# Optimization experiments

Hardware: AMD Instinct MI355X
Metric: run time of the kernel (lower is better)

Reference implementation:

```python
import jax, jax.numpy as jnp
import numpy as np

D = 20            # doc / proto-action feature dim (hard-coded via .view(slate_size, 20))
SLATE = 5
K = 100           # neighbors per slate element
N_DOCS = 1_000_000
HID = 256
SLOPE = 0.01      # F.leaky_relu default negative slope


def setup_inputs() -> dict:
    key = jax.random.key(0)
    ks = jax.random.split(key, 6)
    def lin_w(k, out_d, in_d):
        # kaiming-ish scale, matches torch Linear init magnitude roughly
        return jax.random.uniform(k, (out_d, in_d), jnp.float32, -1.0, 1.0) / np.sqrt(in_d)
    return {
        "input_state": jax.random.normal(ks[0], (D,), jnp.float32),
        "candidate_docs": jax.random.normal(ks[1], (N_DOCS, D), jnp.float32),
        "W1": lin_w(ks[2], HID, D),
        "b1": jnp.zeros((HID,), jnp.float32),
        "W2": lin_w(ks[3], HID, HID),
        "b2": jnp.zeros((HID,), jnp.float32),
        "W3": lin_w(ks[4], SLATE * D, HID),
        "b3": jnp.zeros((SLATE * D,), jnp.float32),
    }


def reference(input_state, candidate_docs, W1, b1, W2, b2, W3, b3):
    # --- actor policy net: Linear -> leaky_relu, x3 (leaky_relu also on output, as in source) ---
    x = input_state
    for W, b in ((W1, b1), (W2, b2), (W3, b3)):
        x = jax.nn.leaky_relu(x @ W.T + b, negative_slope=SLOPE)
    proto_slate = x.reshape(SLATE, D)                       # [slate, 20]

    # --- per-slate-element L2 distance to every candidate doc, vectorized ---
    # dists[s, n] = ||candidate_docs[n] - proto_slate[s]||_2
    diff = candidate_docs[None, :, :] - proto_slate[:, None, :]   # [slate, N, 20]
    dists = jnp.sqrt(jnp.sum(diff * diff, axis=-1))               # [slate, N]

    # top-k smallest distances (replaces full argsort + slice in the source)
    _, idx = jax.lax.top_k(-dists, K)                             # [slate, K]
    indices_tensor = idx.reshape(-1)                              # [slate*K], concat order as in source
    candidates_tensor = candidate_docs[indices_tensor]            # [slate*K, 20]
    return candidates_tensor, indices_tensor
```

## Files before the change

kernel.cpp:

```cpp
#include <hip/hip_runtime.h>
#include <stdint.h>

#define DDIM    20
#define SLATE   5
#define KSEL    100
#define HID     256
#define SAMPN   16384
#define NSH     8
#define SHCAP   1024
#define RCAP    8192
#define STP     128
#define OUT_IDX_OFF (SLATE * KSEL * DDIM)

#define WS_PROTO   0
#define WS_PROTOF  1024
#define WS_TP2     1536
#define WS_TM2     1556
#define WS_THI     1576
#define WS_SHCNT   1600
#define WS_STRICT  4160
#define WS_CNT2    6720
#define WS_ZEND    7040
#define WS_SKEYS   8192
#define WS_CAND    172032
#define WS_CAND2   335872
#define WS_STD2    499712
#define WS_STIX    540672
#define WS_STLEN   561152

__device__ __forceinline__ double dleaky(double x) { return x >= 0.0 ? x : 0.01 * x; }

__device__ __forceinline__ double calc_d2(const float* doc, const double* p) {
    double acc = 0.0;
#pragma unroll
    for (int i = 0; i < DDIM; ++i) {
        double d = (double)doc[i] - p[i];
        acc = fma(d, d, acc);
    }
    return acc;
}

__device__ __forceinline__ void load_doc(const float* __restrict__ docs,
                                         size_t n, float* doc) {
    const float4* dp = (const float4*)(docs + n * DDIM);
    float4 v0 = dp[0], v1 = dp[1], v2 = dp[2], v3 = dp[3], v4 = dp[4];
    doc[0] = v0.x; doc[1] = v0.y; doc[2] = v0.z; doc[3] = v0.w;
    doc[4] = v1.x; doc[5] = v1.y; doc[6] = v1.z; doc[7] = v1.w;
    doc[8] = v2.x; doc[9] = v2.y; doc[10] = v2.z; doc[11] = v2.w;
    doc[12] = v3.x; doc[13] = v3.y; doc[14] = v3.z; doc[15] = v3.w;
    doc[16] = v4.x; doc[17] = v4.y; doc[18] = v4.z; doc[19] = v4.w;
}

__device__ __forceinline__ int slate_use_primary(
    const unsigned* __restrict__ shardCnt, const unsigned* __restrict__ strictSh,
    int s) {
    unsigned strictTot = 0; bool ovf = false;
    for (int sh = 0; sh < NSH; ++sh) {
        if (shardCnt[(sh * SLATE + s) * 16] > SHCAP) ovf = true;
        strictTot += strictSh[(sh * SLATE + s) * 16];
    }
    return (strictTot >= KSEL) && !ovf;
}

__global__ __launch_bounds__(256) void mlp_kernel(
    const float* __restrict__ x0,
    const float* __restrict__ W1, const float* __restrict__ b1,
    const float* __restrict__ W2, const float* __restrict__ b2,
    const float* __restrict__ W3, const float* __restrict__ b3,
    double* __restrict__ proto, float* __restrict__ protof,
    unsigned* __restrict__ zeroBase) {
    __shared__ double xs[DDIM];
    __shared__ double h1[HID];
    __shared__ double h2[HID];
    int t = threadIdx.x;
    for (int i = t; i < 1360; i += 256) zeroBase[i] = 0u;
    if (t < DDIM) xs[t] = (double)x0[t];
    __syncthreads();
    {
        double acc = 0.0;
#pragma unroll
        for (int i = 0; i < DDIM; ++i) acc = fma(xs[i], (double)W1[t * DDIM + i], acc);
        acc += (double)b1[t];
        h1[t] = dleaky(acc);
    }
    __syncthreads();
    {
        double acc = 0.0;
        for (int i = 0; i < HID; ++i) acc = fma(h1[i], (double)W2[t * HID + i], acc);
        acc += (double)b2[t];
        h2[t] = dleaky(acc);
    }
    __syncthreads();
    if (t < SLATE * DDIM) {
        double acc = 0.0;
        for (int i = 0; i < HID; ++i) acc = fma(h2[i], (double)W3[t * HID + i], acc);
        acc += (double)b3[t];
        double v = dleaky(acc);
        proto[t] = v;
        protof[t] = (float)v;
    }
}

__global__ __launch_bounds__(256) void sample_keys_kernel(
    const float* __restrict__ docs, const double* __restrict__ proto,
    unsigned short* __restrict__ skeys, int N) {
    __shared__ double ps[SLATE * DDIM];
    int t = threadIdx.x;
    if (t < SLATE * DDIM) ps[t] = proto[t];
    __syncthreads();
    int i = blockIdx.x * 256 + t;
    if (i >= SAMPN || i >= N) return;
    float doc[DDIM];
    load_doc(docs, (size_t)i, doc);
#pragma unroll
    for (int s = 0; s < SLATE; ++s) {
        double d2 = calc_d2(doc, ps + s * DDIM);
        skeys[s * SAMPN + i] = (unsigned short)(__float_as_uint((float)d2) >> 16);
    }
}

__global__ __launch_bounds__(1024) void select_kernel(
    const unsigned short* __restrict__ skeys,
    unsigned short* __restrict__ Tp2, unsigned short* __restrict__ Tm2,
    unsigned short* __restrict__ Thi) {
    int s = blockIdx.x, t = threadIdx.x;
    int lane = t & 63, w = t >> 6;
    __shared__ unsigned wsum[2][16];
    const unsigned* kp = (const unsigned*)(skeys + (size_t)s * SAMPN);
    unsigned kw[8];
#pragma unroll
    for (int j = 0; j < 8; ++j) kw[j] = kp[j * 1024 + t];

    unsigned X10 = 0, X100 = 0;
    int buf = 0;
    for (int b = 15; b >= 0; --b) {
        unsigned p10 = X10 | (1u << b), p100 = X100 | (1u << b);
        int c10 = 0, c100 = 0;
#pragma unroll
        for (int j = 0; j < 8; ++j) {
            unsigned lo = kw[j] & 0xffffu, hi = kw[j] >> 16;
            c10  += (lo < p10)  + (hi < p10);
            c100 += (lo < p100) + (hi < p100);
        }
#pragma unroll
        for (int off = 32; off; off >>= 1) {
            c10  += __shfl_down(c10, off);
            c100 += __shfl_down(c100, off);
        }
        if (lane == 0) wsum[buf][w] = (unsigned)c10 | ((unsigned)c100 << 16);
        __syncthreads();
        unsigned t10 = 0, t100 = 0;
        for (int i = 0; i < 16; ++i) {
            unsigned v = wsum[buf][i];
            t10 += v & 0xffffu; t100 += v >> 16;
        }
        if ((int)t10 < 10)   X10 = p10;
        if ((int)t100 < 100) X100 = p100;
        buf ^= 1;
    }
    if (t == 0) {
        unsigned tp = X10 + 2u; if (tp > 65535u) tp = 65535u;
        Tp2[s] = (unsigned short)tp;
        Tm2[s] = (unsigned short)(X10 >= 2u ? X10 - 2u : 0u);
        Thi[s] = (unsigned short)X100;
    }
}

__global__ __launch_bounds__(256) void compact1_kernel(
    const float* __restrict__ docs, const float* __restrict__ protof,
    const unsigned short* __restrict__ Tp2, const unsigned short* __restrict__ Tm2,
    unsigned* __restrict__ shardCnt, unsigned* __restrict__ strictSh,
    unsigned* __restrict__ candIdx, int N) {
    __shared__ float psf[SLATE * DDIM];
    __shared__ unsigned short ktp[SLATE], ktm[SLATE];
    int t = threadIdx.x;
    if (t < SLATE * DDIM) psf[t] = protof[t];
    if (t < SLATE) { ktp[t] = Tp2[t]; ktm[t] = Tm2[t]; }
    __syncthreads();

    int n = blockIdx.x * 256 + t;
    bool dv = n < N;
    int lane = t & 63;
    int sh = blockIdx.x & (NSH - 1);

    float doc[DDIM];
    if (dv) load_doc(docs, (size_t)n, doc);
    else {
#pragma unroll
        for (int i = 0; i < DDIM; ++i) doc[i] = 0.f;
    }
    float acc[SLATE] = {0.f, 0.f, 0.f, 0.f, 0.f};
#pragma unroll
    for (int i = 0; i < DDIM; ++i) {
        float dvi = doc[i];
#pragma unroll
        for (int s = 0; s < SLATE; ++s) {
            float d = dvi - psf[s * DDIM + i];
            acc[s] = fmaf(d, d, acc[s]);
        }
    }
#pragma unroll
    for (int s = 0; s < SLATE; ++s) {
        unsigned k32 = __float_as_uint(acc[s]) >> 16;
        bool hit = dv && k32 <= (unsigned)ktp[s];
        unsigned long long ms = __ballot(dv && k32 <= (unsigned)ktm[s]);
        if (ms) {
            int ldr = __ffsll(ms) - 1;
            if (lane == ldr)
                atomicAdd(&strictSh[(sh * SLATE + s) * 16], (unsigned)__popcll(ms));
        }
        unsigned long long mh = __ballot(hit);
        if (mh) {
            int ldr = __ffsll(mh) - 1;
            unsigned base = 0;
            if (lane == ldr)
                base = atomicAdd(&shardCnt[(sh * SLATE + s) * 16], (unsigned)__popcll(mh));
            base = __shfl(base, ldr);
            if (hit) {
                unsigned pos = base + (unsigned)__popcll(mh & ((1ull << lane) - 1ull));
                if (pos < SHCAP)
                    candIdx[((size_t)(s * NSH + sh)) * SHCAP + pos] = (unsigned)n;
            }
        }
    }
}

__global__ __launch_bounds__(256) void compact2_kernel(
    const float* __restrict__ docs, const double* __restrict__ proto,
    const unsigned short* __restrict__ Thi,
    const unsigned* __restrict__ shardCnt, const unsigned* __restrict__ strictSh,
    unsigned* __restrict__ cnt2, unsigned* __restrict__ candIdx2, int N) {
    __shared__ int act[SLATE];
    __shared__ int anyAct;
    __shared__ double ps[SLATE * DDIM];
    __shared__ unsigned short kt[SLATE];
    int t = threadIdx.x;
    if (t == 0) {
        int any = 0;
        for (int s = 0; s < SLATE; ++s) {
            int a = slate_use_primary(shardCnt, strictSh, s) ? 0 : 1;
            act[s] = a; any |= a;
        }
        anyAct = any;
    }
    __syncthreads();
    if (!anyAct) return;

    if (t < SLATE) kt[t] = Thi[t];
    if (t < SLATE * DDIM) ps[t] = proto[t];
    __syncthreads();
    for (int n = blockIdx.x * 256 + t; n < N; n += gridDim.x * 256) {
        float doc[DDIM];
        load_doc(docs, (size_t)n, doc);
        for (int s = 0; s < SLATE; ++s) {
            if (!act[s]) continue;
            double d2 = calc_d2(doc, ps + s * DDIM);
            unsigned key = __float_as_uint((float)d2) >> 16;
            if (key <= (unsigned)kt[s]) {
                unsigned pos = atomicAdd(&cnt2[s * 16], 1u);
                if (pos < RCAP) candIdx2[(size_t)s * RCAP + pos] = (unsigned)n;
            }
        }
    }
}

__global__ __launch_bounds__(256) void shard_rank_kernel(
    const float* __restrict__ docs, const double* __restrict__ proto,
    const unsigned* __restrict__ shardCnt, const unsigned* __restrict__ strictSh,
    const unsigned* __restrict__ cnt2,
    const unsigned* __restrict__ candIdx, const unsigned* __restrict__ candIdx2,
    double* __restrict__ stD2, unsigned* __restrict__ stIx,
    unsigned* __restrict__ stLen, int N) {
    int sh = blockIdx.x, s = blockIdx.y;
    int t = threadIdx.x;
    __shared__ double ld[SHCAP];
    __shared__ unsigned li[SHCAP];
    __shared__ double ps[DDIM];
    __shared__ double outD2[KSEL];
    __shared__ unsigned outIx[KSEL];
    __shared__ unsigned c_s;
    __shared__ const unsigned* src_s;
    if (t < DDIM) ps[t] = proto[s * DDIM + t];
    if (t == 0) {
        if (slate_use_primary(shardCnt, strictSh, s)) {
            unsigned c = shardCnt[(sh * SLATE + s) * 16];
            if (c > SHCAP) c = SHCAP;
            c_s = c;
            src_s = candIdx + ((size_t)(s * NSH + sh)) * SHCAP;
        } else {
            unsigned c2 = cnt2[s * 16]; if (c2 > RCAP) c2 = RCAP;
            unsigned L = (c2 + NSH - 1) / NSH;
            unsigned lo = sh * L, hi = lo + L;
            if (lo > c2) lo = c2;
            if (hi > c2) hi = c2;
            c_s = hi - lo;
            src_s = candIdx2 + (size_t)s * RCAP + lo;
        }
    }
    __syncthreads();
    unsigned c = c_s;
    const unsigned* src = src_s;

    for (unsigned i = t; i < c; i += 256) {
        unsigned idx = src[i];
        li[i] = idx;
        float doc[DDIM];
        load_doc(docs, (size_t)idx, doc);
        ld[i] = calc_d2(doc, ps);
    }
    __syncthreads();

    for (unsigned e = t; e < c; e += 256) {
        double de = ld[e]; unsigned ie = li[e];
        unsigned rank = 0;
        for (unsigned j = 0; j < c; ++j) {
            double dj = ld[j]; unsigned ij = li[j];
            rank += (dj < de) || (dj == de && ij < ie);
        }
        if (rank < KSEL) { outD2[rank] = de; outIx[rank] = ie; }
    }
    __syncthreads();

    unsigned L = c < KSEL ? c : KSEL;
    size_t base = (size_t)(s * NSH + sh) * STP;
    for (unsigned r = t; r < L; r += 256) {
        stD2[base + r] = outD2[r];
        stIx[base + r] = outIx[r];
    }
    if (t == 0) stLen[s * NSH + sh] = L;
}

__global__ __launch_bounds__(1024) void merge_kernel(
    const float* __restrict__ docs,
    const double* __restrict__ stD2, const unsigned* __restrict__ stIx,
    const unsigned* __restrict__ stLen, float* __restrict__ out) {
    int s = blockIdx.x, t = threadIdx.x;
    __shared__ double md[NSH * KSEL];
    __shared__ unsigned mi[NSH * KSEL];
    __shared__ unsigned Ls[NSH], offs[NSH + 1];
    __shared__ unsigned sel[KSEL];
    if (t < NSH) Ls[t] = stLen[s * NSH + t];
    __syncthreads();
    if (t == 0) {
        unsigned o = 0;
        for (int sh = 0; sh < NSH; ++sh) { offs[sh] = o; o += Ls[sh]; }
        offs[NSH] = o;
    }
    __syncthreads();
    for (int sh = 0; sh < NSH; ++sh) {
        unsigned L = Ls[sh];
        for (unsigned i = t; i < L; i += 1024) {
            md[sh * KSEL + i] = stD2[(size_t)(s * NSH + sh) * STP + i];
            mi[sh * KSEL + i] = stIx[(size_t)(s * NSH + sh) * STP + i];
        }
    }
    __syncthreads();

    unsigned S = offs[NSH];
    for (unsigned e = t; e < S; e += 1024) {
        int sh = 0;
        while (e >= offs[sh + 1]) ++sh;
        unsigned i = e - offs[sh];
        double xd = md[sh * KSEL + i];
        unsigned xi = mi[sh * KSEL + i];
        unsigned rank = i;
        for (int so = 0; so < NSH; ++so) {
            if (so == sh) continue;
            unsigned lo = 0, hi = Ls[so];
            while (lo < hi) {
                unsigned mid = (lo + hi) >> 1;
                double dj = md[so * KSEL + mid];
                unsigned ij = mi[so * KSEL + mid];
                bool less = (dj < xd) || (dj == xd && ij < xi);
                if (less) lo = mid + 1; else hi = mid;
            }
            rank += lo;
        }
        if (rank < KSEL) sel[rank] = xi;
    }
    __syncthreads();

    if (t < KSEL) out[(size_t)OUT_IDX_OFF + s * KSEL + t] = (float)sel[t];
    for (int pos = t; pos < KSEL * DDIM; pos += 1024) {
        int r = pos / DDIM, c = pos % DDIM;
        out[((size_t)s * KSEL + r) * DDIM + c] = docs[(size_t)sel[r] * DDIM + c];
    }
}

extern "C" void kernel_launch(void* const* d_in, const int* in_sizes, int n_in,
                              void* d_out, int out_size, void* d_ws, size_t ws_size,
                              hipStream_t stream) {
    const float* x0   = (const float*)d_in[0];
    const float* docs = (const float*)d_in[1];
    const float* W1   = (const float*)d_in[2];
    const float* b1   = (const float*)d_in[3];
    const float* W2   = (const float*)d_in[4];
    const float* b2   = (const float*)d_in[5];
    const float* W3   = (const float*)d_in[6];
    const float* b3   = (const float*)d_in[7];
    int N = in_sizes[1] / DDIM;

    char* ws = (char*)d_ws;
    double*         proto    = (double*)(ws + WS_PROTO);
    float*          protof   = (float*)(ws + WS_PROTOF);
    unsigned short* Tp2      = (unsigned short*)(ws + WS_TP2);
    unsigned short* Tm2      = (unsigned short*)(ws + WS_TM2);
    unsigned short* Thi      = (unsigned short*)(ws + WS_THI);
    unsigned*       shardCnt = (unsigned*)(ws + WS_SHCNT);
    unsigned*       strictSh = (unsigned*)(ws + WS_STRICT);
    unsigned*       cnt2     = (unsigned*)(ws + WS_CNT2);
    unsigned short* skeys    = (unsigned short*)(ws + WS_SKEYS);
    unsigned*       candIdx  = (unsigned*)(ws + WS_CAND);
    unsigned*       candIdx2 = (unsigned*)(ws + WS_CAND2);
    double*         stD2     = (double*)(ws + WS_STD2);
    unsigned*       stIx     = (unsigned*)(ws + WS_STIX);
    unsigned*       stLen    = (unsigned*)(ws + WS_STLEN);

    mlp_kernel<<<1, 256, 0, stream>>>(x0, W1, b1, W2, b2, W3, b3,
                                      proto, protof, shardCnt);
    sample_keys_kernel<<<SAMPN / 256, 256, 0, stream>>>(docs, proto, skeys, N);
    select_kernel<<<SLATE, 1024, 0, stream>>>(skeys, Tp2, Tm2, Thi);

    int nb = (N + 255) / 256;
    compact1_kernel<<<nb, 256, 0, stream>>>(docs, protof, Tp2, Tm2,
                                            shardCnt, strictSh, candIdx, N);
    compact2_kernel<<<1024, 256, 0, stream>>>(docs, proto, Thi, shardCnt, strictSh,
                                              cnt2, candIdx2, N);
    shard_rank_kernel<<<dim3(NSH, SLATE), 256, 0, stream>>>(
        docs, proto, shardCnt, strictSh, cnt2, candIdx, candIdx2,
        stD2, stIx, stLen, N);
    merge_kernel<<<SLATE, 1024, 0, stream>>>(docs, stD2, stIx, stLen,
                                             (float*)d_out);
}
```

Measured before the change: 103.4 us.

## Fuse the seven-kernel pipeline into one cooperative persistent kernel with grid syncs

Replaces the chain of seven kernel launches (MLP, sampling, threshold select, two compaction passes, shard ranking, merge) with a single cooperative kernel. Phases are separated by grid.sync, and the shared memory for each phase is overlaid through a union. The MLP is recomputed redundantly in each sampling block so the separate single-block MLP launch disappears. Compaction becomes a grid-stride loop over a grid sized from the occupancy query, capped at 1024 blocks. This removes launch gaps and serial tiny kernels at the cost of grid-wide barriers, partial occupancy during the small phases, and a fallback path if the cooperative launch fails.

```diff
diff --git a/kernel.cpp b/kernel.cpp
--- a/kernel.cpp
+++ b/kernel.cpp
@@ -1,5 +1,8 @@
 #include <hip/hip_runtime.h>
+#include <hip/hip_cooperative_groups.h>
 #include <stdint.h>
+
+namespace cg = cooperative_groups;
 
 #define DDIM    20
 #define SLATE   5
@@ -61,6 +64,316 @@
     }
     return (strictTot >= KSEL) && !ovf;
 }
+
+
+struct SmMlp  { double xs[DDIM]; double h1[HID]; double h2[HID]; double ps[SLATE * DDIM]; };
+struct SmSel  { unsigned wsum[2][4]; };
+struct SmCmp  { float psf[SLATE * DDIM]; unsigned short ktp[SLATE]; unsigned short ktm[SLATE]; };
+struct SmRec  { double ps[SLATE * DDIM]; unsigned short kt[SLATE]; int act[SLATE]; int anyAct; };
+struct SmRank { double ld[SHCAP]; double outD2[KSEL]; double ps[DDIM];
+                unsigned li[SHCAP]; unsigned outIx[KSEL];
+                unsigned c; const unsigned* src; };
+struct SmMrg  { double md[NSH * KSEL]; unsigned mi[NSH * KSEL];
+                unsigned Ls[NSH]; unsigned offs[NSH + 1]; unsigned sel[KSEL]; };
+union SmU { SmMlp mlp; SmSel sel; SmCmp cmp; SmRec rec; SmRank rank; SmMrg mrg; };
+
+__global__ __launch_bounds__(256, 4) void fused_kernel(
+    const float* __restrict__ x0, const float* __restrict__ docs,
+    const float* __restrict__ W1, const float* __restrict__ b1,
+    const float* __restrict__ W2, const float* __restrict__ b2,
+    const float* __restrict__ W3, const float* __restrict__ b3,
+    double* __restrict__ proto, float* __restrict__ protof,
+    unsigned short* __restrict__ Tp2, unsigned short* __restrict__ Tm2,
+    unsigned short* __restrict__ Thi,
+    unsigned* __restrict__ shardCnt, unsigned* __restrict__ strictSh,
+    unsigned* __restrict__ cnt2, unsigned short* __restrict__ skeys,
+    unsigned* __restrict__ candIdx, unsigned* __restrict__ candIdx2,
+    double* __restrict__ stD2, unsigned* __restrict__ stIx,
+    unsigned* __restrict__ stLen, float* __restrict__ out, int N) {
+    cg::grid_group grid = cg::this_grid();
+    const int bid  = blockIdx.x;
+    const int t    = threadIdx.x;
+    const int nblk = gridDim.x;
+    __shared__ SmU sm;
+
+    if (bid < SAMPN / 256) {
+        SmMlp& M = sm.mlp;
+        if (t < DDIM) M.xs[t] = (double)x0[t];
+        __syncthreads();
+        {
+            double acc = 0.0;
+#pragma unroll
+            for (int i = 0; i < DDIM; ++i) acc = fma(M.xs[i], (double)W1[t * DDIM + i], acc);
+            acc += (double)b1[t];
+            M.h1[t] = dleaky(acc);
+        }
+        __syncthreads();
+        {
+            double acc = 0.0;
+            for (int i = 0; i < HID; ++i) acc = fma(M.h1[i], (double)W2[t * HID + i], acc);
+            acc += (double)b2[t];
+            M.h2[t] = dleaky(acc);
+        }
+        __syncthreads();
+        if (t < SLATE * DDIM) {
+            double acc = 0.0;
+            for (int i = 0; i < HID; ++i) acc = fma(M.h2[i], (double)W3[t * HID + i], acc);
+            acc += (double)b3[t];
+            double v = dleaky(acc);
+            M.ps[t] = v;
+            if (bid == 0) { proto[t] = v; protof[t] = (float)v; }
+        }
+        __syncthreads();
+        int i = bid * 256 + t;
+        if (i < N) {
+            float doc[DDIM];
+            load_doc(docs, (size_t)i, doc);
+#pragma unroll
+            for (int s = 0; s < SLATE; ++s) {
+                double d2 = calc_d2(doc, M.ps + s * DDIM);
+                skeys[s * SAMPN + i] = (unsigned short)(__float_as_uint((float)d2) >> 16);
+            }
+        }
+    } else if (bid == SAMPN / 256) {
+        for (int i = t; i < 1360; i += 256) shardCnt[i] = 0u;
+    }
+    grid.sync();
+
+    if (bid < SLATE) {
+        const int s = bid, lane = t & 63, w = t >> 6;
+        const unsigned* kp = (const unsigned*)(skeys + (size_t)s * SAMPN);
+        unsigned kw[32];
+#pragma unroll
+        for (int j = 0; j < 32; ++j) kw[j] = kp[j * 256 + t];
+
+        unsigned X10 = 0, X100 = 0;
+        int buf = 0;
+        for (int b = 15; b >= 0; --b) {
+            unsigned p10 = X10 | (1u << b), p100 = X100 | (1u << b);
+            int c10 = 0, c100 = 0;
+#pragma unroll
+            for (int j = 0; j < 32; ++j) {
+                unsigned lo = kw[j] & 0xffffu, hi = kw[j] >> 16;
+                c10  += (lo < p10)  + (hi < p10);
+                c100 += (lo < p100) + (hi < p100);
+            }
+#pragma unroll
+            for (int off = 32; off; off >>= 1) {
+                c10  += __shfl_down(c10, off);
+                c100 += __shfl_down(c100, off);
+            }
+            if (lane == 0) sm.sel.wsum[buf][w] = (unsigned)c10 | ((unsigned)c100 << 16);
+            __syncthreads();
+            unsigned t10 = 0, t100 = 0;
+            for (int i = 0; i < 4; ++i) {
+                unsigned v = sm.sel.wsum[buf][i];
+                t10 += v & 0xffffu; t100 += v >> 16;
+            }
+            if ((int)t10 < 10)   X10 = p10;
+            if ((int)t100 < 100) X100 = p100;
+            buf ^= 1;
+        }
+        if (t == 0) {
+            unsigned tp = X10 + 2u; if (tp > 65535u) tp = 65535u;
+            Tp2[s] = (unsigned short)tp;
+            Tm2[s] = (unsigned short)(X10 >= 2u ? X10 - 2u : 0u);
+            Thi[s] = (unsigned short)X100;
+        }
+    }
+    grid.sync();
+
+    {
+        SmCmp& C = sm.cmp;
+        if (t < SLATE * DDIM) C.psf[t] = protof[t];
+        if (t < SLATE) { C.ktp[t] = Tp2[t]; C.ktm[t] = Tm2[t]; }
+        __syncthreads();
+        const int lane = t & 63;
+        const int sh = bid & (NSH - 1);
+        for (int base = bid * 256; base < N; base += nblk * 256) {
+            int n = base + t;
+            bool dv = n < N;
+            float doc[DDIM];
+            if (dv) load_doc(docs, (size_t)n, doc);
+            else {
+#pragma unroll
+                for (int i = 0; i < DDIM; ++i) doc[i] = 0.f;
+            }
+            float acc[SLATE] = {0.f, 0.f, 0.f, 0.f, 0.f};
+#pragma unroll
+            for (int i = 0; i < DDIM; ++i) {
+                float dvi = doc[i];
+#pragma unroll
+                for (int s = 0; s < SLATE; ++s) {
+                    float d = dvi - C.psf[s * DDIM + i];
+                    acc[s] = fmaf(d, d, acc[s]);
+                }
+            }
+#pragma unroll
+            for (int s = 0; s < SLATE; ++s) {
+                unsigned k32 = __float_as_uint(acc[s]) >> 16;
+                bool hit = dv && k32 <= (unsigned)C.ktp[s];
+                unsigned long long ms = __ballot(dv && k32 <= (unsigned)C.ktm[s]);
+                if (ms) {
+                    int ldr = __ffsll(ms) - 1;
+                    if (lane == ldr)
+                        atomicAdd(&strictSh[(sh * SLATE + s) * 16], (unsigned)__popcll(ms));
+                }
+                unsigned long long mh = __ballot(hit);
+                if (mh) {
+                    int ldr = __ffsll(mh) - 1;
+                    unsigned base2 = 0;
+                    if (lane == ldr)
+                        base2 = atomicAdd(&shardCnt[(sh * SLATE + s) * 16], (unsigned)__popcll(mh));
+                    base2 = __shfl(base2, ldr);
+                    if (hit) {
+                        unsigned pos = base2 + (unsigned)__popcll(mh & ((1ull << lane) - 1ull));
+                        if (pos < SHCAP)
+                            candIdx[((size_t)(s * NSH + sh)) * SHCAP + pos] = (unsigned)n;
+                    }
+                }
+            }
+        }
+    }
+    grid.sync();
+
+    {
+        SmRec& R = sm.rec;
+        if (t == 0) {
+            int any = 0;
+            for (int s = 0; s < SLATE; ++s) {
+                int a = slate_use_primary(shardCnt, strictSh, s) ? 0 : 1;
+                R.act[s] = a; any |= a;
+            }
+            R.anyAct = any;
+        }
+        __syncthreads();
+        if (R.anyAct) {
+            if (t < SLATE) R.kt[t] = Thi[t];
+            if (t < SLATE * DDIM) R.ps[t] = proto[t];
+            __syncthreads();
+            for (int n = bid * 256 + t; n < N; n += nblk * 256) {
+                float doc[DDIM];
+                load_doc(docs, (size_t)n, doc);
+                for (int s = 0; s < SLATE; ++s) {
+                    if (!R.act[s]) continue;
+                    double d2 = calc_d2(doc, R.ps + s * DDIM);
+                    unsigned key = __float_as_uint((float)d2) >> 16;
+                    if (key <= (unsigned)R.kt[s]) {
+                        unsigned pos = atomicAdd(&cnt2[s * 16], 1u);
+                        if (pos < RCAP) candIdx2[(size_t)s * RCAP + pos] = (unsigned)n;
+                    }
+                }
+            }
+            grid.sync();
+        }
+    }
+
+    if (bid < NSH * SLATE) {
+        const int sh = bid & (NSH - 1), s = bid >> 3;
+        SmRank& K = sm.rank;
+        if (t < DDIM) K.ps[t] = proto[s * DDIM + t];
+        if (t == 0) {
+            if (slate_use_primary(shardCnt, strictSh, s)) {
+                unsigned c = shardCnt[(sh * SLATE + s) * 16];
+                if (c > SHCAP) c = SHCAP;
+                K.c = c;
+                K.src = candIdx + ((size_t)(s * NSH + sh)) * SHCAP;
+            } else {
+                unsigned c2 = cnt2[s * 16]; if (c2 > RCAP) c2 = RCAP;
+                unsigned L = (c2 + NSH - 1) / NSH;
+                unsigned lo = sh * L, hi = lo + L;
+                if (lo > c2) lo = c2;
+                if (hi > c2) hi = c2;
+                K.c = hi - lo;
+                K.src = candIdx2 + (size_t)s * RCAP + lo;
+            }
+        }
+        __syncthreads();
+        unsigned c = K.c;
+        const unsigned* src = K.src;
+
+        for (unsigned i = t; i < c; i += 256) {
+            unsigned idx = src[i];
+            K.li[i] = idx;
+            float doc[DDIM];
+            load_doc(docs, (size_t)idx, doc);
+            K.ld[i] = calc_d2(doc, K.ps);
+        }
+        __syncthreads();
+
+        for (unsigned e = t; e < c; e += 256) {
+            double de = K.ld[e]; unsigned ie = K.li[e];
+            unsigned rank = 0;
+            for (unsigned j = 0; j < c; ++j) {
+                double dj = K.ld[j]; unsigned ij = K.li[j];
+                rank += (dj < de) || (dj == de && ij < ie);
+            }
+            if (rank < KSEL) { K.outD2[rank] = de; K.outIx[rank] = ie; }
+        }
+        __syncthreads();
+
+        unsigned L = c < KSEL ? c : KSEL;
+        size_t base = (size_t)(s * NSH + sh) * STP;
+        for (unsigned r = t; r < L; r += 256) {
+            stD2[base + r] = K.outD2[r];
+            stIx[base + r] = K.outIx[r];
+        }
+        if (t == 0) stLen[s * NSH + sh] = L;
+    }
+    grid.sync();
+
+    if (bid < SLATE) {
+        const int s = bid;
+        SmMrg& G = sm.mrg;
+        if (t < NSH) G.Ls[t] = stLen[s * NSH + t];
+        __syncthreads();
+        if (t == 0) {
+            unsigned o = 0;
+            for (int sh = 0; sh < NSH; ++sh) { G.offs[sh] = o; o += G.Ls[sh]; }
+            G.offs[NSH] = o;
+        }
+        __syncthreads();
+        for (int sh = 0; sh < NSH; ++sh) {
+            unsigned L = G.Ls[sh];
+            for (unsigned i = t; i < L; i += 256) {
+                G.md[sh * KSEL + i] = stD2[(size_t)(s * NSH + sh) * STP + i];
+                G.mi[sh * KSEL + i] = stIx[(size_t)(s * NSH + sh) * STP + i];
+            }
+        }
+        __syncthreads();
+
+        unsigned S = G.offs[NSH];
+        for (unsigned e = t; e < S; e += 256) {
+            int sh = 0;
+            while (e >= G.offs[sh + 1]) ++sh;
+            unsigned i = e - G.offs[sh];
+            double xd = G.md[sh * KSEL + i];
+            unsigned xi = G.mi[sh * KSEL + i];
+            unsigned rank = i;
+            for (int so = 0; so < NSH; ++so) {
+                if (so == sh) continue;
+                unsigned lo = 0, hi = G.Ls[so];
+                while (lo < hi) {
+                    unsigned mid = (lo + hi) >> 1;
+                    double dj = G.md[so * KSEL + mid];
+                    unsigned ij = G.mi[so * KSEL + mid];
+                    bool less = (dj < xd) || (dj == xd && ij < xi);
+                    if (less) lo = mid + 1; else hi = mid;
+                }
+                rank += lo;
+            }
+            if (rank < KSEL) G.sel[rank] = xi;
+        }
+        __syncthreads();
+
+        if (t < KSEL) out[(size_t)OUT_IDX_OFF + s * KSEL + t] = (float)G.sel[t];
+        for (int pos = t; pos < KSEL * DDIM; pos += 256) {
+            int r = pos / DDIM, c = pos % DDIM;
+            out[((size_t)s * KSEL + r) * DDIM + c] = docs[(size_t)G.sel[r] * DDIM + c];
+        }
+    }
+}
+
 
 __global__ __launch_bounds__(256) void mlp_kernel(
     const float* __restrict__ x0,
@@ -415,20 +728,61 @@
     double*         stD2     = (double*)(ws + WS_STD2);
     unsigned*       stIx     = (unsigned*)(ws + WS_STIX);
     unsigned*       stLen    = (unsigned*)(ws + WS_STLEN);
-
-    mlp_kernel<<<1, 256, 0, stream>>>(x0, W1, b1, W2, b2, W3, b3,
-                                      proto, protof, shardCnt);
-    sample_keys_kernel<<<SAMPN / 256, 256, 0, stream>>>(docs, proto, skeys, N);
-    select_kernel<<<SLATE, 1024, 0, stream>>>(skeys, Tp2, Tm2, Thi);
-
-    int nb = (N + 255) / 256;
-    compact1_kernel<<<nb, 256, 0, stream>>>(docs, protof, Tp2, Tm2,
-                                            shardCnt, strictSh, candIdx, N);
-    compact2_kernel<<<1024, 256, 0, stream>>>(docs, proto, Thi, shardCnt, strictSh,
-                                              cnt2, candIdx2, N);
-    shard_rank_kernel<<<dim3(NSH, SLATE), 256, 0, stream>>>(
-        docs, proto, shardCnt, strictSh, cnt2, candIdx, candIdx2,
-        stD2, stIx, stLen, N);
-    merge_kernel<<<SLATE, 1024, 0, stream>>>(docs, stD2, stIx, stLen,
-                                             (float*)d_out);
-}
+    float*          outp     = (float*)d_out;
+
+    static int g_nblk = -1;
+    if (g_nblk == -1) {
+        int per_cu = 0;
+        if (hipOccupancyMaxActiveBlocksPerMultiprocessor(&per_cu, fused_kernel, 256, 0)
+                != hipSuccess || per_cu <= 0)
+            per_cu = 0;
+        int ncu = 256;
+        int dev = 0;
+        hipDeviceProp_t prop;
+        if (hipGetDevice(&dev) == hipSuccess &&
+            hipGetDeviceProperties(&prop, dev) == hipSuccess &&
+            prop.multiProcessorCount > 0)
+            ncu = prop.multiProcessorCount;
+        long cap = (long)per_cu * (long)ncu;
+        int nb = cap >= 1024 ? 1024 : (int)cap;
+        nb &= ~7;
+        g_nblk = (nb >= 72) ? nb : 0;
+    }
+
+    bool done = false;
+    if (g_nblk > 0) {
+        void* args[] = { (void*)&x0, (void*)&docs, (void*)&W1, (void*)&b1,
+                         (void*)&W2, (void*)&b2, (void*)&W3, (void*)&b3,
+                         (void*)&proto, (void*)&protof,
+                         (void*)&Tp2, (void*)&Tm2, (void*)&Thi,
+                         (void*)&shardCnt, (void*)&strictSh, (void*)&cnt2,
+                         (void*)&skeys, (void*)&candIdx, (void*)&candIdx2,
+                         (void*)&stD2, (void*)&stIx, (void*)&stLen,
+                         (void*)&outp, (void*)&N };
+        hipError_t e = hipLaunchCooperativeKernel((const void*)fused_kernel,
+                                                  dim3(g_nblk), dim3(256),
+                                                  args, 0, stream);
+        if (e == hipSuccess) {
+            done = true;
+        } else {
+            (void)hipGetLastError();
+            g_nblk = 0;
+        }
+    }
+
+    if (!done) {
+        mlp_kernel<<<1, 256, 0, stream>>>(x0, W1, b1, W2, b2, W3, b3,
+                                          proto, protof, shardCnt);
+        sample_keys_kernel<<<SAMPN / 256, 256, 0, stream>>>(docs, proto, skeys, N);
+        select_kernel<<<SLATE, 1024, 0, stream>>>(skeys, Tp2, Tm2, Thi);
+        int nb = (N + 255) / 256;
+        compact1_kernel<<<nb, 256, 0, stream>>>(docs, protof, Tp2, Tm2,
+                                                shardCnt, strictSh, candIdx, N);
+        compact2_kernel<<<1024, 256, 0, stream>>>(docs, proto, Thi, shardCnt, strictSh,
+                                                  cnt2, candIdx2, N);
+        shard_rank_kernel<<<dim3(NSH, SLATE), 256, 0, stream>>>(
+            docs, proto, shardCnt, strictSh, cnt2, candIdx, candIdx2,
+            stD2, stIx, stLen, N);
+        merge_kernel<<<SLATE, 1024, 0, stream>>>(docs, stD2, stIx, stLen, outp);
+    }
+}
```

Measured after the change: 329.3 us. 218% more time.

## Fuse MLP with sampling and merge rank stages into one per-slate kernel

Applied to the files above, without the earlier changes.

Each sampling block now recomputes the MLP redundantly so the separate MLP launch disappears, with an extra block doing the counter zeroing. The fallback full-scan compaction, the per-shard ranking and the merge are replaced by one 1024-thread kernel per slate. It gathers all primary candidates and ranks them with a chunked all-pairs comparison, templated on how many candidates each thread owns. This cuts launches and global round-trips, but every block repeats the MLP work, and the fallback path now scans all N docs from only 5 blocks.

```diff
diff --git a/kernel.cpp b/kernel.cpp
--- a/kernel.cpp
+++ b/kernel.cpp
@@ -1,5 +1,6 @@
 #include <hip/hip_runtime.h>
 #include <stdint.h>
+#include <math.h>
 
 #define DDIM    20
 #define SLATE   5
@@ -9,7 +10,7 @@
 #define NSH     8
 #define SHCAP   1024
 #define RCAP    8192
-#define STP     128
+#define CHUNK   2048
 #define OUT_IDX_OFF (SLATE * KSEL * DDIM)
 
 #define WS_PROTO   0
@@ -24,9 +25,6 @@
 #define WS_SKEYS   8192
 #define WS_CAND    172032
 #define WS_CAND2   335872
-#define WS_STD2    499712
-#define WS_STIX    540672
-#define WS_STLEN   561152
 
 __device__ __forceinline__ double dleaky(double x) { return x >= 0.0 ? x : 0.01 * x; }
 
@@ -62,18 +60,22 @@
     return (strictTot >= KSEL) && !ovf;
 }
 
-__global__ __launch_bounds__(256) void mlp_kernel(
-    const float* __restrict__ x0,
+__global__ __launch_bounds__(256) void mlp_sample_kernel(
+    const float* __restrict__ x0, const float* __restrict__ docs,
     const float* __restrict__ W1, const float* __restrict__ b1,
     const float* __restrict__ W2, const float* __restrict__ b2,
     const float* __restrict__ W3, const float* __restrict__ b3,
     double* __restrict__ proto, float* __restrict__ protof,
-    unsigned* __restrict__ zeroBase) {
+    unsigned short* __restrict__ skeys, unsigned* __restrict__ zeroBase, int N) {
+    const int bid = blockIdx.x, t = threadIdx.x;
+    if (bid == SAMPN / 256) {
+        for (int i = t; i < 1360; i += 256) zeroBase[i] = 0u;
+        return;
+    }
     __shared__ double xs[DDIM];
     __shared__ double h1[HID];
     __shared__ double h2[HID];
-    int t = threadIdx.x;
-    for (int i = t; i < 1360; i += 256) zeroBase[i] = 0u;
+    __shared__ double ps[SLATE * DDIM];
     if (t < DDIM) xs[t] = (double)x0[t];
     __syncthreads();
     {
@@ -96,26 +98,19 @@
         for (int i = 0; i < HID; ++i) acc = fma(h2[i], (double)W3[t * HID + i], acc);
         acc += (double)b3[t];
         double v = dleaky(acc);
-        proto[t] = v;
-        protof[t] = (float)v;
-    }
-}
-
-__global__ __launch_bounds__(256) void sample_keys_kernel(
-    const float* __restrict__ docs, const double* __restrict__ proto,
-    unsigned short* __restrict__ skeys, int N) {
-    __shared__ double ps[SLATE * DDIM];
-    int t = threadIdx.x;
-    if (t < SLATE * DDIM) ps[t] = proto[t];
-    __syncthreads();
-    int i = blockIdx.x * 256 + t;
-    if (i >= SAMPN || i >= N) return;
-    float doc[DDIM];
-    load_doc(docs, (size_t)i, doc);
-#pragma unroll
-    for (int s = 0; s < SLATE; ++s) {
-        double d2 = calc_d2(doc, ps + s * DDIM);
-        skeys[s * SAMPN + i] = (unsigned short)(__float_as_uint((float)d2) >> 16);
+        ps[t] = v;
+        if (bid == 0) { proto[t] = v; protof[t] = (float)v; }
+    }
+    __syncthreads();
+    int i = bid * 256 + t;
+    if (i < SAMPN && i < N) {
+        float doc[DDIM];
+        load_doc(docs, (size_t)i, doc);
+#pragma unroll
+        for (int s = 0; s < SLATE; ++s) {
+            double d2 = calc_d2(doc, ps + s * DDIM);
+            skeys[s * SAMPN + i] = (unsigned short)(__float_as_uint((float)d2) >> 16);
+        }
     }
 }
 
@@ -225,165 +220,117 @@
     }
 }
 
-__global__ __launch_bounds__(256) void compact2_kernel(
+template<int NOWN>
+__device__ __forceinline__ void rank_select(
+    const float* __restrict__ docs, const unsigned* __restrict__ lst,
+    unsigned ctot, const double* ps, double* ld, unsigned* li,
+    unsigned* outIx, int t) {
+    double   myD2[NOWN];
+    unsigned myIx[NOWN];
+    unsigned myRank[NOWN];
+#pragma unroll
+    for (int k = 0; k < NOWN; ++k) {
+        unsigned e = (unsigned)t + 1024u * (unsigned)k;
+        myD2[k] = INFINITY; myIx[k] = 0xffffffffu; myRank[k] = 0u;
+        if (e < ctot) {
+            unsigned idx = lst[e];
+            float doc[DDIM];
+            load_doc(docs, (size_t)idx, doc);
+            myIx[k] = idx;
+            myD2[k] = calc_d2(doc, ps);
+        }
+    }
+    for (unsigned c0 = 0; c0 < ctot; c0 += CHUNK) {
+        unsigned cn = (ctot - c0) < CHUNK ? (ctot - c0) : CHUNK;
+        __syncthreads();
+        for (unsigned j = t; j < cn; j += 1024) {
+            unsigned idx = lst[c0 + j];
+            float doc[DDIM];
+            load_doc(docs, (size_t)idx, doc);
+            li[j] = idx;
+            ld[j] = calc_d2(doc, ps);
+        }
+        __syncthreads();
+        for (unsigned j = 0; j < cn; ++j) {
+            double dj = ld[j]; unsigned ij = li[j];
+#pragma unroll
+            for (int k = 0; k < NOWN; ++k)
+                myRank[k] += ((dj < myD2[k]) || (dj == myD2[k] && ij < myIx[k])) ? 1u : 0u;
+        }
+    }
+    __syncthreads();
+#pragma unroll
+    for (int k = 0; k < NOWN; ++k)
+        if (myRank[k] < KSEL) outIx[myRank[k]] = myIx[k];
+}
+
+__global__ __launch_bounds__(1024) void rank_merge_kernel(
     const float* __restrict__ docs, const double* __restrict__ proto,
     const unsigned short* __restrict__ Thi,
     const unsigned* __restrict__ shardCnt, const unsigned* __restrict__ strictSh,
-    unsigned* __restrict__ cnt2, unsigned* __restrict__ candIdx2, int N) {
-    __shared__ int act[SLATE];
-    __shared__ int anyAct;
-    __shared__ double ps[SLATE * DDIM];
-    __shared__ unsigned short kt[SLATE];
-    int t = threadIdx.x;
-    if (t == 0) {
-        int any = 0;
-        for (int s = 0; s < SLATE; ++s) {
-            int a = slate_use_primary(shardCnt, strictSh, s) ? 0 : 1;
-            act[s] = a; any |= a;
-        }
-        anyAct = any;
-    }
-    __syncthreads();
-    if (!anyAct) return;
-
-    if (t < SLATE) kt[t] = Thi[t];
-    if (t < SLATE * DDIM) ps[t] = proto[t];
-    __syncthreads();
-    for (int n = blockIdx.x * 256 + t; n < N; n += gridDim.x * 256) {
-        float doc[DDIM];
-        load_doc(docs, (size_t)n, doc);
-        for (int s = 0; s < SLATE; ++s) {
-            if (!act[s]) continue;
-            double d2 = calc_d2(doc, ps + s * DDIM);
-            unsigned key = __float_as_uint((float)d2) >> 16;
-            if (key <= (unsigned)kt[s]) {
-                unsigned pos = atomicAdd(&cnt2[s * 16], 1u);
-                if (pos < RCAP) candIdx2[(size_t)s * RCAP + pos] = (unsigned)n;
-            }
-        }
-    }
-}
-
-__global__ __launch_bounds__(256) void shard_rank_kernel(
-    const float* __restrict__ docs, const double* __restrict__ proto,
-    const unsigned* __restrict__ shardCnt, const unsigned* __restrict__ strictSh,
-    const unsigned* __restrict__ cnt2,
-    const unsigned* __restrict__ candIdx, const unsigned* __restrict__ candIdx2,
-    double* __restrict__ stD2, unsigned* __restrict__ stIx,
-    unsigned* __restrict__ stLen, int N) {
-    int sh = blockIdx.x, s = blockIdx.y;
-    int t = threadIdx.x;
-    __shared__ double ld[SHCAP];
-    __shared__ unsigned li[SHCAP];
-    __shared__ double ps[DDIM];
-    __shared__ double outD2[KSEL];
+    const unsigned* __restrict__ candIdx, unsigned* __restrict__ scratch,
+    float* __restrict__ out, int N) {
+    const int s = blockIdx.x, t = threadIdx.x;
+    __shared__ double   ps[DDIM];
+    __shared__ double   ld[CHUNK];
+    __shared__ unsigned li[CHUNK];
+    __shared__ unsigned offs[NSH + 1];
     __shared__ unsigned outIx[KSEL];
-    __shared__ unsigned c_s;
-    __shared__ const unsigned* src_s;
+    __shared__ unsigned ctot_s;
+    __shared__ int      prim_s;
+    __shared__ unsigned rcnt;
     if (t < DDIM) ps[t] = proto[s * DDIM + t];
     if (t == 0) {
-        if (slate_use_primary(shardCnt, strictSh, s)) {
-            unsigned c = shardCnt[(sh * SLATE + s) * 16];
-            if (c > SHCAP) c = SHCAP;
-            c_s = c;
-            src_s = candIdx + ((size_t)(s * NSH + sh)) * SHCAP;
-        } else {
-            unsigned c2 = cnt2[s * 16]; if (c2 > RCAP) c2 = RCAP;
-            unsigned L = (c2 + NSH - 1) / NSH;
-            unsigned lo = sh * L, hi = lo + L;
-            if (lo > c2) lo = c2;
-            if (hi > c2) hi = c2;
-            c_s = hi - lo;
-            src_s = candIdx2 + (size_t)s * RCAP + lo;
-        }
-    }
-    __syncthreads();
-    unsigned c = c_s;
-    const unsigned* src = src_s;
-
-    for (unsigned i = t; i < c; i += 256) {
-        unsigned idx = src[i];
-        li[i] = idx;
-        float doc[DDIM];
-        load_doc(docs, (size_t)idx, doc);
-        ld[i] = calc_d2(doc, ps);
-    }
-    __syncthreads();
-
-    for (unsigned e = t; e < c; e += 256) {
-        double de = ld[e]; unsigned ie = li[e];
-        unsigned rank = 0;
-        for (unsigned j = 0; j < c; ++j) {
-            double dj = ld[j]; unsigned ij = li[j];
-            rank += (dj < de) || (dj == de && ij < ie);
-        }
-        if (rank < KSEL) { outD2[rank] = de; outIx[rank] = ie; }
-    }
-    __syncthreads();
-
-    unsigned L = c < KSEL ? c : KSEL;
-    size_t base = (size_t)(s * NSH + sh) * STP;
-    for (unsigned r = t; r < L; r += 256) {
-        stD2[base + r] = outD2[r];
-        stIx[base + r] = outIx[r];
-    }
-    if (t == 0) stLen[s * NSH + sh] = L;
-}
-
-__global__ __launch_bounds__(1024) void merge_kernel(
-    const float* __restrict__ docs,
-    const double* __restrict__ stD2, const unsigned* __restrict__ stIx,
-    const unsigned* __restrict__ stLen, float* __restrict__ out) {
-    int s = blockIdx.x, t = threadIdx.x;
-    __shared__ double md[NSH * KSEL];
-    __shared__ unsigned mi[NSH * KSEL];
-    __shared__ unsigned Ls[NSH], offs[NSH + 1];
-    __shared__ unsigned sel[KSEL];
-    if (t < NSH) Ls[t] = stLen[s * NSH + t];
-    __syncthreads();
-    if (t == 0) {
-        unsigned o = 0;
-        for (int sh = 0; sh < NSH; ++sh) { offs[sh] = o; o += Ls[sh]; }
-        offs[NSH] = o;
-    }
-    __syncthreads();
-    for (int sh = 0; sh < NSH; ++sh) {
-        unsigned L = Ls[sh];
-        for (unsigned i = t; i < L; i += 1024) {
-            md[sh * KSEL + i] = stD2[(size_t)(s * NSH + sh) * STP + i];
-            mi[sh * KSEL + i] = stIx[(size_t)(s * NSH + sh) * STP + i];
-        }
-    }
-    __syncthreads();
-
-    unsigned S = offs[NSH];
-    for (unsigned e = t; e < S; e += 1024) {
-        int sh = 0;
-        while (e >= offs[sh + 1]) ++sh;
-        unsigned i = e - offs[sh];
-        double xd = md[sh * KSEL + i];
-        unsigned xi = mi[sh * KSEL + i];
-        unsigned rank = i;
-        for (int so = 0; so < NSH; ++so) {
-            if (so == sh) continue;
-            unsigned lo = 0, hi = Ls[so];
-            while (lo < hi) {
-                unsigned mid = (lo + hi) >> 1;
-                double dj = md[so * KSEL + mid];
-                unsigned ij = mi[so * KSEL + mid];
-                bool less = (dj < xd) || (dj == xd && ij < xi);
-                if (less) lo = mid + 1; else hi = mid;
+        int p = slate_use_primary(shardCnt, strictSh, s);
+        prim_s = p;
+        rcnt = 0u;
+        if (p) {
+            unsigned o = 0;
+            for (int sh = 0; sh < NSH; ++sh) {
+                offs[sh] = o;
+                o += shardCnt[(sh * SLATE + s) * 16];
             }
-            rank += lo;
-        }
-        if (rank < KSEL) sel[rank] = xi;
-    }
-    __syncthreads();
-
-    if (t < KSEL) out[(size_t)OUT_IDX_OFF + s * KSEL + t] = (float)sel[t];
+            offs[NSH] = o;
+            ctot_s = o;
+        }
+    }
+    __syncthreads();
+    unsigned* lst = scratch + (size_t)s * RCAP;
+    unsigned ctot;
+    if (prim_s) {
+        ctot = ctot_s;
+        for (unsigned e = t; e < ctot; e += 1024) {
+            int sh = 0;
+            while (e >= offs[sh + 1]) ++sh;
+            lst[e] = candIdx[((size_t)(s * NSH + sh)) * SHCAP + (e - offs[sh])];
+        }
+    } else {
+        unsigned kt = Thi[s];
+        for (int n = t; n < N; n += 1024) {
+            float doc[DDIM];
+            load_doc(docs, (size_t)n, doc);
+            double d2 = calc_d2(doc, ps);
+            unsigned key = __float_as_uint((float)d2) >> 16;
+            if (key <= kt) {
+                unsigned pos = atomicAdd(&rcnt, 1u);
+                if (pos < RCAP) lst[pos] = (unsigned)n;
+            }
+        }
+        __syncthreads();
+        ctot = rcnt < RCAP ? rcnt : RCAP;
+    }
+    __syncthreads();
+
+    if (ctot <= 1024u)      rank_select<1>(docs, lst, ctot, ps, ld, li, outIx, t);
+    else if (ctot <= 2048u) rank_select<2>(docs, lst, ctot, ps, ld, li, outIx, t);
+    else if (ctot <= 4096u) rank_select<4>(docs, lst, ctot, ps, ld, li, outIx, t);
+    else                    rank_select<8>(docs, lst, ctot, ps, ld, li, outIx, t);
+    __syncthreads();
+
+    if (t < KSEL) out[(size_t)OUT_IDX_OFF + s * KSEL + t] = (float)outIx[t];
     for (int pos = t; pos < KSEL * DDIM; pos += 1024) {
         int r = pos / DDIM, c = pos % DDIM;
-        out[((size_t)s * KSEL + r) * DDIM + c] = docs[(size_t)sel[r] * DDIM + c];
+        out[((size_t)s * KSEL + r) * DDIM + c] = docs[(size_t)outIx[r] * DDIM + c];
     }
 }
 
@@ -408,27 +355,17 @@
     unsigned short* Thi      = (unsigned short*)(ws + WS_THI);
     unsigned*       shardCnt = (unsigned*)(ws + WS_SHCNT);
     unsigned*       strictSh = (unsigned*)(ws + WS_STRICT);
-    unsigned*       cnt2     = (unsigned*)(ws + WS_CNT2);
     unsigned short* skeys    = (unsigned short*)(ws + WS_SKEYS);
     unsigned*       candIdx  = (unsigned*)(ws + WS_CAND);
-    unsigned*       candIdx2 = (unsigned*)(ws + WS_CAND2);
-    double*         stD2     = (double*)(ws + WS_STD2);
-    unsigned*       stIx     = (unsigned*)(ws + WS_STIX);
-    unsigned*       stLen    = (unsigned*)(ws + WS_STLEN);
-
-    mlp_kernel<<<1, 256, 0, stream>>>(x0, W1, b1, W2, b2, W3, b3,
-                                      proto, protof, shardCnt);
-    sample_keys_kernel<<<SAMPN / 256, 256, 0, stream>>>(docs, proto, skeys, N);
+    unsigned*       scratch  = (unsigned*)(ws + WS_CAND2);
+    float*          outp     = (float*)d_out;
+
+    mlp_sample_kernel<<<SAMPN / 256 + 1, 256, 0, stream>>>(
+        x0, docs, W1, b1, W2, b2, W3, b3, proto, protof, skeys, shardCnt, N);
     select_kernel<<<SLATE, 1024, 0, stream>>>(skeys, Tp2, Tm2, Thi);
-
     int nb = (N + 255) / 256;
     compact1_kernel<<<nb, 256, 0, stream>>>(docs, protof, Tp2, Tm2,
                                             shardCnt, strictSh, candIdx, N);
-    compact2_kernel<<<1024, 256, 0, stream>>>(docs, proto, Thi, shardCnt, strictSh,
-                                              cnt2, candIdx2, N);
-    shard_rank_kernel<<<dim3(NSH, SLATE), 256, 0, stream>>>(
-        docs, proto, shardCnt, strictSh, cnt2, candIdx, candIdx2,
-        stD2, stIx, stLen, N);
-    merge_kernel<<<SLATE, 1024, 0, stream>>>(docs, stD2, stIx, stLen,
-                                             (float*)d_out);
-}
+    rank_merge_kernel<<<SLATE, 1024, 0, stream>>>(
+        docs, proto, Thi, shardCnt, strictSh, candIdx, scratch, outp, N);
+}
```

Result: slower. 116.1 us (+12.3%).
